# Kernel optimization log

Hardware: AMD Instinct MI355X
Metric: run time of the kernel (lower is better)

## Reference

```python
import jax, jax.numpy as jnp
import numpy as np

B, S, D, H, DK = 8, 1024, 768, 12, 64


def setup_inputs() -> dict:
    key = jax.random.key(0)
    k1, k2, k3, k4, k5 = jax.random.split(key, 5)
    return {
        "x": jax.random.normal(k1, (B, S, D), dtype=jnp.float32),
        "Wq": jax.random.normal(k2, (H, D, DK), dtype=jnp.float32),
        "Wk": jax.random.normal(k3, (H, D, DK), dtype=jnp.float32),
        "Wv": jax.random.normal(k4, (H, D, DK), dtype=jnp.float32),
        "W": jax.random.normal(k5, (D, D), dtype=jnp.float32),
    }


def reference(x, Wq, Wk, Wv, W):
    # Batched equivalent of the per-head SelfAttention loop + concat + W matmul.
    q = jnp.einsum("bsd,hdk->bhsk", x, Wq)  # [B,H,S,DK]
    k = jnp.einsum("bsd,hdk->bhsk", x, Wk)
    v = jnp.einsum("bsd,hdk->bhsk", x, Wv)
    scale = 1.0 / jnp.sqrt(jnp.asarray(DK, dtype=x.dtype))
    scores = jnp.einsum("bhsk,bhtk->bhst", q, k) * scale  # [B,H,S,S]
    attn = jax.nn.softmax(scores, axis=-1)
    z = jnp.einsum("bhst,bhtk->bhsk", attn, v)  # [B,H,S,DK]
    # concat heads along last dim: [B,S,H*DK]
    z = jnp.transpose(z, (0, 2, 1, 3)).reshape(x.shape[0], x.shape[1], H * DK)
    return jnp.matmul(z, W)  # [B,S,D]
```

## Files before the change

kernel.cpp:

```cpp
#include <hip/hip_runtime.h>

#define Bv 8
#define Sv 1024
#define Dv 768
#define Hv 12
#define DKv 64
#define Mv (Bv*Sv)
#define NQKV (3*Hv*DKv)
#define NQK (2*Hv*DKv)

typedef __attribute__((ext_vector_type(8))) short short8;
typedef __attribute__((ext_vector_type(4))) float f32x4;

__device__ __forceinline__ short f2bf(float f) {
    unsigned u = __builtin_bit_cast(unsigned, f);
    u += 0x7fffu + ((u >> 16) & 1u);
    return (short)(u >> 16);
}
__device__ __forceinline__ float bf2f(short h) {
    return __builtin_bit_cast(float, (unsigned)(unsigned short)h << 16);
}

__device__ __forceinline__ f32x4 mfma16(short8 a, short8 b, f32x4 c) {
    return __builtin_amdgcn_mfma_f32_16x16x32_bf16(a, b, c, 0, 0, 0);
}

__device__ __forceinline__ void gload16(const short* g, const short* l) {
    __builtin_amdgcn_global_load_lds(
        (const __attribute__((address_space(1))) unsigned int*)g,
        (__attribute__((address_space(3))) unsigned int*)(short*)l, 16, 0, 0);
}

__global__ void split_x_kernel(const float* __restrict__ x, short* __restrict__ xh,
                               short* __restrict__ xl) {
    int t = blockIdx.x * 256 + threadIdx.x;
    const float4* f = (const float4*)x + (size_t)t * 2;
    float4 a = f[0], b = f[1];
    float v[8] = {a.x,a.y,a.z,a.w,b.x,b.y,b.z,b.w};
    short8 oh, ol;
#pragma unroll
    for (int k = 0; k < 8; k++) {
        short hi = f2bf(v[k]);
        oh[k] = hi;
        ol[k] = f2bf(v[k] - bf2f(hi));
    }
    *((short8*)xh + t) = oh;
    *((short8*)xl + t) = ol;
}

__global__ void pack_wqkv_kernel(const float* __restrict__ Wq, const float* __restrict__ Wk,
                                 const float* __restrict__ Wv, short* __restrict__ Wh,
                                 short* __restrict__ Wl) {
    int dt = blockIdx.x;
    int h  = blockIdx.y;
    int p  = blockIdx.z;
    const float* S = (p == 0 ? Wq : (p == 1 ? Wk : Wv)) + (size_t)h * Dv * DKv;
    float sc = (p == 0) ? 0.125f : 1.0f;
    __shared__ float lds[64][65];
    int t = threadIdx.x;
    int d0 = dt * 64;
#pragma unroll
    for (int i = 0; i < 4; i++) {
        int v = t + i * 256;
        int r = v >> 4, c4 = v & 15;
        float4 f = *(const float4*)&S[(size_t)(d0 + r) * DKv + c4 * 4];
        lds[r][c4*4+0] = f.x; lds[r][c4*4+1] = f.y; lds[r][c4*4+2] = f.z; lds[r][c4*4+3] = f.w;
    }
    __syncthreads();
#pragma unroll
    for (int i = 0; i < 2; i++) {
        int v = t + i * 256;
        int kk = v >> 3, dl0 = (v & 7) * 8;
        short8 oh, ol;
#pragma unroll
        for (int k = 0; k < 8; k++) {
            float f = lds[dl0 + k][kk] * sc;
            short hi = f2bf(f);
            oh[k] = hi;
            ol[k] = f2bf(f - bf2f(hi));
        }
        size_t base = (size_t)(p*768 + h*64 + kk) * Dv + d0 + dl0;
        *(short8*)&Wh[base] = oh;
        if (p < 2) *(short8*)&Wl[base] = ol;
    }
}

__global__ void transpose_cast_kernel(const float* __restrict__ S, int S_cols,
                                      short* __restrict__ D, int D_ld) {
    int c0 = blockIdx.x * 64, r0 = blockIdx.y * 64;
    __shared__ float lds[64][65];
    int t = threadIdx.x;
#pragma unroll
    for (int i = 0; i < 4; i++) {
        int v = t + i * 256;
        int r = v >> 4, c4 = v & 15;
        float4 f = *(const float4*)&S[(size_t)(r0 + r) * S_cols + c0 + c4 * 4];
        lds[r][c4*4+0] = f.x; lds[r][c4*4+1] = f.y; lds[r][c4*4+2] = f.z; lds[r][c4*4+3] = f.w;
    }
    __syncthreads();
#pragma unroll
    for (int i = 0; i < 2; i++) {
        int v = t + i * 256;
        int oc = v >> 3, rl0 = (v & 7) * 8;
        short8 o;
#pragma unroll
        for (int k = 0; k < 8; k++) o[k] = f2bf(lds[rl0 + k][oc]);
        *(short8*)&D[(size_t)(c0 + oc) * D_ld + r0 + rl0] = o;
    }
}

__global__ void vtrans_kernel(const short* __restrict__ QKVh, short* __restrict__ Vt) {
    int sc = blockIdx.x;
    int bh = blockIdx.y;
    int b = bh / Hv, h = bh % Hv;
    __shared__ __align__(16) short lds[64][72];
    int t = threadIdx.x;
    int s0 = sc * 64;
#pragma unroll
    for (int i = 0; i < 2; i++) {
        int v = t + i * 256;
        int sl = v >> 3, c0 = (v & 7) * 8;
        short8 xv = *(const short8*)&QKVh[(size_t)(b*Sv + s0 + sl) * NQKV + NQK + h*DKv + c0];
        *(short8*)&lds[sl][c0] = xv;
    }
    __syncthreads();
#pragma unroll
    for (int i = 0; i < 2; i++) {
        int v = t + i * 256;
        int dk = v >> 3, tl0 = (v & 7) * 8;
        short8 o;
#pragma unroll
        for (int k = 0; k < 8; k++) o[k] = lds[tl0 + k][dk];
        *(short8*)&Vt[(size_t)(bh*64 + dk) * Sv + s0 + tl0] = o;
    }
}

__device__ __forceinline__ void swz_xy(int n, int& xbl, int& ybl) {
    int cx = n & 7, k = n >> 3;
    ybl = cx + 8 * (k & 7);
    xbl = k >> 3;
}

__global__ __launch_bounds__(256, 4) void gemm1_kernel(const short* __restrict__ xh,
                                                       const short* __restrict__ xl,
                                                       const short* __restrict__ Wh,
                                                       const short* __restrict__ Wl,
                                                       short* __restrict__ QKVh,
                                                       short* __restrict__ QKVl) {
    int xbl, ybl;
    swz_xy(blockIdx.x, xbl, ybl);
    int m0 = ybl * 128, n0 = xbl * 128;
    bool isv = (n0 >= NQK);
    int KT = isv ? 24 : 72;
    __shared__ __align__(16) short lA[2][4096];
    __shared__ __align__(16) short lB[2][4096];
    int tid = threadIdx.x, lane = tid & 63, w = tid >> 6;
    int wr = w >> 1, wc = w & 1;
    int li = lane & 15, g = lane >> 4;
    f32x4 zero = {0.f, 0.f, 0.f, 0.f};
    f32x4 acc[4][4];
#pragma unroll
    for (int i = 0; i < 4; i++)
#pragma unroll
        for (int j = 0; j < 4; j++) acc[i][j] = zero;

    int e0 = tid * 8;
    int sr0 = e0 >> 5;
    int sc0 = ((e0 >> 3) & 3) ^ ((sr0 >> 1) & 3);
    int sr1 = sr0 + 64;
    int sc1 = ((e0 >> 3) & 3) ^ ((sr1 >> 1) & 3);

    auto stage = [&](int t, int buf) {
        int seg = (t >= 48) ? 2 : (t >= 24 ? 1 : 0);
        int kk = (t - seg * 24) * 32;
        const short* Ab = (seg == 2) ? xl : xh;
        const short* Bb = (seg == 1) ? Wl : Wh;
        gload16(Ab + (size_t)(m0 + sr0) * Dv + kk + sc0 * 8, &lA[buf][w * 512]);
        gload16(Bb + (size_t)(n0 + sr0) * Dv + kk + sc0 * 8, &lB[buf][w * 512]);
        gload16(Ab + (size_t)(m0 + sr1) * Dv + kk + sc1 * 8, &lA[buf][2048 + w * 512]);
        gload16(Bb + (size_t)(n0 + sr1) * Dv + kk + sc1 * 8, &lB[buf][2048 + w * 512]);
    };

    stage(0, 0);
    stage(1, 1);

    for (int t = 0; t < KT; t++) {
        int cur = t & 1;
        if (t + 1 < KT) asm volatile("s_waitcnt vmcnt(4)" ::: "memory");
        else            asm volatile("s_waitcnt vmcnt(0)" ::: "memory");
        __builtin_amdgcn_s_barrier();
        __builtin_amdgcn_sched_barrier(0);
        short8 a[4], bb[4];
#pragma unroll
        for (int mi = 0; mi < 4; mi++) {
            int row = wr*64 + mi*16 + li;
            a[mi] = *(const short8*)&lA[cur][row * 32 + ((g ^ ((row >> 1) & 3)) << 3)];
        }
#pragma unroll
        for (int ni = 0; ni < 4; ni++) {
            int row = wc*64 + ni*16 + li;
            bb[ni] = *(const short8*)&lB[cur][row * 32 + ((g ^ ((row >> 1) & 3)) << 3)];
        }
#pragma unroll
        for (int mi = 0; mi < 4; mi++)
#pragma unroll
            for (int ni = 0; ni < 4; ni++)
                acc[mi][ni] = mfma16(a[mi], bb[ni], acc[mi][ni]);
        __builtin_amdgcn_sched_barrier(0);
        __builtin_amdgcn_s_barrier();
        __builtin_amdgcn_sched_barrier(0);
        if (t + 2 < KT) stage(t + 2, cur);
    }
#pragma unroll
    for (int mi = 0; mi < 4; mi++)
#pragma unroll
        for (int ni = 0; ni < 4; ni++)
#pragma unroll
            for (int j = 0; j < 4; j++) {
                int row = m0 + wr*64 + mi*16 + g*4 + j;
                int col = n0 + wc*64 + ni*16 + li;
                float v = acc[mi][ni][j];
                short hi = f2bf(v);
                QKVh[(size_t)row * NQKV + col] = hi;
                if (!isv) QKVl[(size_t)row * NQK + col] = f2bf(v - bf2f(hi));
            }
}

__global__ __launch_bounds__(256, 4) void gemm2_kernel(const short* __restrict__ A,
                                                       const short* __restrict__ Bt,
                                                       float* __restrict__ C) {
    int xbl, ybl;
    swz_xy(blockIdx.x, xbl, ybl);
    int m0 = ybl * 128, n0 = xbl * 128;
    __shared__ __align__(16) short lA[2][4096];
    __shared__ __align__(16) short lB[2][4096];
    int tid = threadIdx.x, lane = tid & 63, w = tid >> 6;
    int wr = w >> 1, wc = w & 1;
    int li = lane & 15, g = lane >> 4;
    f32x4 zero = {0.f, 0.f, 0.f, 0.f};
    f32x4 acc[4][4];
#pragma unroll
    for (int i = 0; i < 4; i++)
#pragma unroll
        for (int j = 0; j < 4; j++) acc[i][j] = zero;

    int e0 = tid * 8;
    int sr0 = e0 >> 5;
    int sc0 = ((e0 >> 3) & 3) ^ ((sr0 >> 1) & 3);
    int sr1 = sr0 + 64;
    int sc1 = ((e0 >> 3) & 3) ^ ((sr1 >> 1) & 3);

    auto stage = [&](int t, int buf) {
        int kk = t * 32;
        gload16(A  + (size_t)(m0 + sr0) * Dv + kk + sc0 * 8, &lA[buf][w * 512]);
        gload16(Bt + (size_t)(n0 + sr0) * Dv + kk + sc0 * 8, &lB[buf][w * 512]);
        gload16(A  + (size_t)(m0 + sr1) * Dv + kk + sc1 * 8, &lA[buf][2048 + w * 512]);
        gload16(Bt + (size_t)(n0 + sr1) * Dv + kk + sc1 * 8, &lB[buf][2048 + w * 512]);
    };

    stage(0, 0);
    stage(1, 1);

    for (int t = 0; t < 24; t++) {
        int cur = t & 1;
        if (t + 1 < 24) asm volatile("s_waitcnt vmcnt(4)" ::: "memory");
        else            asm volatile("s_waitcnt vmcnt(0)" ::: "memory");
        __builtin_amdgcn_s_barrier();
        __builtin_amdgcn_sched_barrier(0);
        short8 a[4], bb[4];
#pragma unroll
        for (int mi = 0; mi < 4; mi++) {
            int row = wr*64 + mi*16 + li;
            a[mi] = *(const short8*)&lA[cur][row * 32 + ((g ^ ((row >> 1) & 3)) << 3)];
        }
#pragma unroll
        for (int ni = 0; ni < 4; ni++) {
            int row = wc*64 + ni*16 + li;
            bb[ni] = *(const short8*)&lB[cur][row * 32 + ((g ^ ((row >> 1) & 3)) << 3)];
        }
#pragma unroll
        for (int mi = 0; mi < 4; mi++)
#pragma unroll
            for (int ni = 0; ni < 4; ni++)
                acc[mi][ni] = mfma16(a[mi], bb[ni], acc[mi][ni]);
        __builtin_amdgcn_sched_barrier(0);
        __builtin_amdgcn_s_barrier();
        __builtin_amdgcn_sched_barrier(0);
        if (t + 2 < 24) stage(t + 2, cur);
    }
#pragma unroll
    for (int mi = 0; mi < 4; mi++)
#pragma unroll
        for (int ni = 0; ni < 4; ni++)
#pragma unroll
            for (int j = 0; j < 4; j++) {
                int row = m0 + wr*64 + mi*16 + g*4 + j;
                int col = n0 + wc*64 + ni*16 + li;
                C[(size_t)row * Dv + col] = acc[mi][ni][j];
            }
}

__global__ __launch_bounds__(512, 6) void attn_kernel(const short* __restrict__ QKVh,
                                                      const short* __restrict__ QKVl,
                                                      const short* __restrict__ Vt,
                                                      short* __restrict__ Z) {
    int n = blockIdx.x;
    int j2 = n >> 3;
    int bh = (n & 7) + 8 * (j2 >> 3);
    int qb = j2 & 7;
    int b = bh / Hv, h = bh % Hv;
    int tid = threadIdx.x, lane = tid & 63, w = tid >> 6;
    int li = lane & 15, g = lane >> 4;

    __shared__ __align__(16) short Kh[64 * 64];
    __shared__ __align__(16) short Kl[64 * 64];
    __shared__ __align__(16) short Vs[64 * 64];
    __shared__ __align__(16) short P[8][1024];
    char* Pw = (char*)&P[w][0];
    const char* Khc = (const char*)Kh;
    const char* Klc = (const char*)Kl;
    const char* Vsc = (const char*)Vs;

    int qr0 = qb * 128 + w * 16;
    const short* qhr = QKVh + (size_t)(b*Sv + qr0 + li) * NQKV + h * DKv;
    const short* qlr = QKVl + (size_t)(b*Sv + qr0 + li) * NQK  + h * DKv;
    short8 qh0 = *(const short8*)(qhr + g * 8);
    short8 qh1 = *(const short8*)(qhr + 32 + g * 8);
    short8 ql0 = *(const short8*)(qlr + g * 8);
    short8 ql1 = *(const short8*)(qlr + 32 + g * 8);

    const short* Khb = QKVh + (size_t)(b*Sv) * NQKV + Hv*DKv + h*DKv;
    const short* Klb = QKVl + (size_t)(b*Sv) * NQK  + Hv*DKv + h*DKv;
    const short* Vbase = Vt + (size_t)(bh * 64) * Sv;

    int srow = w * 8 + (lane >> 3);
    int scs  = (lane & 7) ^ (srow & 7);

    float mm = -1e30f, ll = 0.f;
    f32x4 zero = {0.f, 0.f, 0.f, 0.f};
    f32x4 acc[4];
#pragma unroll
    for (int ni = 0; ni < 4; ni++) acc[ni] = zero;

    for (int t = 0; t < 16; t++) {
        int t0 = t * 64;
        gload16(Khb + (size_t)(t0 + srow) * NQKV + scs * 8, &Kh[w * 512]);
        gload16(Klb + (size_t)(t0 + srow) * NQK  + scs * 8, &Kl[w * 512]);
        gload16(Vbase + (size_t)srow * Sv + t0 + scs * 8,   &Vs[w * 512]);
        __syncthreads();

        f32x4 s[4];
#pragma unroll
        for (int tn = 0; tn < 4; tn++) {
            int row = tn * 16 + li;
            int rb = row * 128, rs = (row & 7) << 4;
            short8 kh0 = *(const short8*)(Khc + rb + ((g << 4) ^ rs));
            short8 kh1 = *(const short8*)(Khc + rb + ((64 + (g << 4)) ^ rs));
            short8 kl0 = *(const short8*)(Klc + rb + ((g << 4) ^ rs));
            short8 kl1 = *(const short8*)(Klc + rb + ((64 + (g << 4)) ^ rs));
            f32x4 z = mfma16(kh0, qh0, zero);
            z = mfma16(kh1, qh1, z);
            z = mfma16(kl0, qh0, z);
            z = mfma16(kl1, qh1, z);
            z = mfma16(kh0, ql0, z);
            z = mfma16(kh1, ql1, z);
            s[tn] = z;
        }
        float rm = s[0][0];
#pragma unroll
        for (int tn = 0; tn < 4; tn++)
#pragma unroll
            for (int jj = 0; jj < 4; jj++) rm = fmaxf(rm, s[tn][jj]);
        rm = fmaxf(rm, __shfl_xor(rm, 16));
        rm = fmaxf(rm, __shfl_xor(rm, 32));
        float mn = fmaxf(mm, rm);
        float sfu = __expf(mm - mn);
        float p[4][4];
        float rs2 = 0.f;
#pragma unroll
        for (int tn = 0; tn < 4; tn++)
#pragma unroll
            for (int jj = 0; jj < 4; jj++) { p[tn][jj] = __expf(s[tn][jj] - mn); rs2 += p[tn][jj]; }
        rs2 += __shfl_xor(rs2, 16);
        rs2 += __shfl_xor(rs2, 32);
        ll = ll * sfu + rs2;
        mm = mn;

        float sfq[4];
#pragma unroll
        for (int jj = 0; jj < 4; jj++) sfq[jj] = __shfl(sfu, g * 4 + jj);
#pragma unroll
        for (int ni = 0; ni < 4; ni++)
#pragma unroll
            for (int jj = 0; jj < 4; jj++) acc[ni][jj] *= sfq[jj];

#pragma unroll
        for (int tn = 0; tn < 4; tn++) {
            unsigned lo, hi;
            asm("v_cvt_pk_bf16_f32 %0, %1, %2" : "=v"(lo) : "v"(p[tn][0]), "v"(p[tn][1]));
            asm("v_cvt_pk_bf16_f32 %0, %1, %2" : "=v"(hi) : "v"(p[tn][2]), "v"(p[tn][3]));
            unsigned long long pk = (unsigned long long)lo | ((unsigned long long)hi << 32);
            int off = (li * 128 + tn * 32 + g * 8) ^ ((li & 7) << 4);
            *(unsigned long long*)(Pw + off) = pk;
        }
#pragma unroll
        for (int kt = 0; kt < 2; kt++) {
            int roff = (li * 128 + kt * 64 + g * 16) ^ ((li & 7) << 4);
            short8 ap = *(const short8*)(Pw + roff);
#pragma unroll
            for (int ni = 0; ni < 4; ni++) {
                int dk = ni * 16 + li;
                int vb = dk * 128 + ((((kt * 4 + g) << 4)) ^ ((dk & 7) << 4));
                short8 bv = *(const short8*)(Vsc + vb);
                acc[ni] = mfma16(ap, bv, acc[ni]);
            }
        }
        __syncthreads();
    }
    float inv = 1.f / ll;
    float invq[4];
#pragma unroll
    for (int jj = 0; jj < 4; jj++) invq[jj] = __shfl(inv, g * 4 + jj);
#pragma unroll
    for (int ni = 0; ni < 4; ni++)
#pragma unroll
        for (int jj = 0; jj < 4; jj++) {
            int row = b*Sv + qr0 + g*4 + jj;
            int col = h*DKv + ni*16 + li;
            Z[(size_t)row * Dv + col] = f2bf(acc[ni][jj] * invq[jj]);
        }
}

extern "C" void kernel_launch(void* const* d_in, const int* in_sizes, int n_in,
                              void* d_out, int out_size, void* d_ws, size_t ws_size,
                              hipStream_t stream) {
    const float* x  = (const float*)d_in[0];
    const float* Wq = (const float*)d_in[1];
    const float* Wk = (const float*)d_in[2];
    const float* Wv = (const float*)d_in[3];
    const float* W  = (const float*)d_in[4];
    float* out = (float*)d_out;

    short* xh   = (short*)d_ws;
    short* xl   = xh   + (size_t)Mv * Dv;
    short* Wh   = xl   + (size_t)Mv * Dv;
    short* Wl   = Wh   + (size_t)NQKV * Dv;
    short* W2T  = Wl   + (size_t)NQKV * Dv;
    short* QKVh = W2T  + (size_t)Dv * Dv;
    short* QKVl = QKVh + (size_t)Mv * NQKV;
    short* Vt   = QKVl + (size_t)Mv * NQK;
    short* Zb   = Vt   + (size_t)Bv*Hv*DKv * Sv;

    split_x_kernel<<<dim3(Mv * Dv / (256 * 8)), 256, 0, stream>>>(x, xh, xl);
    pack_wqkv_kernel<<<dim3(Dv/64, Hv, 3), 256, 0, stream>>>(Wq, Wk, Wv, Wh, Wl);
    transpose_cast_kernel<<<dim3(Dv/64, Dv/64), 256, 0, stream>>>(W, Dv, W2T, Dv);
    gemm1_kernel<<<dim3((NQKV/128) * (Mv/128)), 256, 0, stream>>>(xh, xl, Wh, Wl, QKVh, QKVl);
    vtrans_kernel<<<dim3(Sv/64, Bv*Hv), 256, 0, stream>>>(QKVh, Vt);
    attn_kernel<<<dim3(768), 512, 0, stream>>>(QKVh, QKVl, Vt, Zb);
    gemm2_kernel<<<dim3((Dv/128) * (Mv/128)), 256, 0, stream>>>(Zb, W2T, out);
}
```

Baseline: 203.4 us.

## Merge prep kernels into one launch and fuse V transpose into QKV GEMM epilogue

Three preprocessing kernels (x hi/lo split, Wqkv packing, W transpose-cast) are merged into one launch that dispatches on block index. The separate V transpose kernel is removed: the QKV GEMM epilogue for V tiles now writes bf16 results straight into the transposed Vt layout as 4-element vectors, so V is never written to QKVh and never re-read. This removes two kernel launches and a full read/write pass over V. In exchange, the Vt stores are narrow 8-byte writes at a stride of one sequence row, which may coalesce worse than the old epilogue stores.

```diff
diff --git a/kernel.cpp b/kernel.cpp
--- a/kernel.cpp
+++ b/kernel.cpp
@@ -10,6 +10,7 @@
 #define NQK (2*Hv*DKv)
 
 typedef __attribute__((ext_vector_type(8))) short short8;
+typedef __attribute__((ext_vector_type(4))) short short4v;
 typedef __attribute__((ext_vector_type(4))) float f32x4;
 
 __device__ __forceinline__ short f2bf(float f) {
@@ -31,107 +32,81 @@
         (__attribute__((address_space(3))) unsigned int*)(short*)l, 16, 0, 0);
 }
 
-__global__ void split_x_kernel(const float* __restrict__ x, short* __restrict__ xh,
-                               short* __restrict__ xl) {
-    int t = blockIdx.x * 256 + threadIdx.x;
-    const float4* f = (const float4*)x + (size_t)t * 2;
-    float4 a = f[0], b = f[1];
-    float v[8] = {a.x,a.y,a.z,a.w,b.x,b.y,b.z,b.w};
-    short8 oh, ol;
-#pragma unroll
-    for (int k = 0; k < 8; k++) {
-        short hi = f2bf(v[k]);
-        oh[k] = hi;
-        ol[k] = f2bf(v[k] - bf2f(hi));
-    }
-    *((short8*)xh + t) = oh;
-    *((short8*)xl + t) = ol;
-}
-
-__global__ void pack_wqkv_kernel(const float* __restrict__ Wq, const float* __restrict__ Wk,
-                                 const float* __restrict__ Wv, short* __restrict__ Wh,
-                                 short* __restrict__ Wl) {
-    int dt = blockIdx.x;
-    int h  = blockIdx.y;
-    int p  = blockIdx.z;
-    const float* S = (p == 0 ? Wq : (p == 1 ? Wk : Wv)) + (size_t)h * Dv * DKv;
-    float sc = (p == 0) ? 0.125f : 1.0f;
+__global__ __launch_bounds__(256) void prep_kernel(const float* __restrict__ x,
+                                                   const float* __restrict__ Wq,
+                                                   const float* __restrict__ Wk,
+                                                   const float* __restrict__ Wv,
+                                                   const float* __restrict__ W,
+                                                   short* __restrict__ xh, short* __restrict__ xl,
+                                                   short* __restrict__ Wh, short* __restrict__ Wl,
+                                                   short* __restrict__ W2T) {
     __shared__ float lds[64][65];
+    int bid = blockIdx.x;
     int t = threadIdx.x;
-    int d0 = dt * 64;
-#pragma unroll
-    for (int i = 0; i < 4; i++) {
-        int v = t + i * 256;
-        int r = v >> 4, c4 = v & 15;
-        float4 f = *(const float4*)&S[(size_t)(d0 + r) * DKv + c4 * 4];
-        lds[r][c4*4+0] = f.x; lds[r][c4*4+1] = f.y; lds[r][c4*4+2] = f.z; lds[r][c4*4+3] = f.w;
-    }
-    __syncthreads();
-#pragma unroll
-    for (int i = 0; i < 2; i++) {
-        int v = t + i * 256;
-        int kk = v >> 3, dl0 = (v & 7) * 8;
+    if (bid < 3072) {
+        int idx = bid * 256 + t;
+        const float4* f = (const float4*)x + (size_t)idx * 2;
+        float4 a = f[0], b = f[1];
+        float v[8] = {a.x,a.y,a.z,a.w,b.x,b.y,b.z,b.w};
         short8 oh, ol;
 #pragma unroll
         for (int k = 0; k < 8; k++) {
-            float f = lds[dl0 + k][kk] * sc;
-            short hi = f2bf(f);
+            short hi = f2bf(v[k]);
             oh[k] = hi;
-            ol[k] = f2bf(f - bf2f(hi));
-        }
-        size_t base = (size_t)(p*768 + h*64 + kk) * Dv + d0 + dl0;
-        *(short8*)&Wh[base] = oh;
-        if (p < 2) *(short8*)&Wl[base] = ol;
-    }
-}
-
-__global__ void transpose_cast_kernel(const float* __restrict__ S, int S_cols,
-                                      short* __restrict__ D, int D_ld) {
-    int c0 = blockIdx.x * 64, r0 = blockIdx.y * 64;
-    __shared__ float lds[64][65];
-    int t = threadIdx.x;
-#pragma unroll
-    for (int i = 0; i < 4; i++) {
-        int v = t + i * 256;
-        int r = v >> 4, c4 = v & 15;
-        float4 f = *(const float4*)&S[(size_t)(r0 + r) * S_cols + c0 + c4 * 4];
-        lds[r][c4*4+0] = f.x; lds[r][c4*4+1] = f.y; lds[r][c4*4+2] = f.z; lds[r][c4*4+3] = f.w;
-    }
-    __syncthreads();
-#pragma unroll
-    for (int i = 0; i < 2; i++) {
-        int v = t + i * 256;
-        int oc = v >> 3, rl0 = (v & 7) * 8;
-        short8 o;
-#pragma unroll
-        for (int k = 0; k < 8; k++) o[k] = f2bf(lds[rl0 + k][oc]);
-        *(short8*)&D[(size_t)(c0 + oc) * D_ld + r0 + rl0] = o;
-    }
-}
-
-__global__ void vtrans_kernel(const short* __restrict__ QKVh, short* __restrict__ Vt) {
-    int sc = blockIdx.x;
-    int bh = blockIdx.y;
-    int b = bh / Hv, h = bh % Hv;
-    __shared__ __align__(16) short lds[64][72];
-    int t = threadIdx.x;
-    int s0 = sc * 64;
-#pragma unroll
-    for (int i = 0; i < 2; i++) {
-        int v = t + i * 256;
-        int sl = v >> 3, c0 = (v & 7) * 8;
-        short8 xv = *(const short8*)&QKVh[(size_t)(b*Sv + s0 + sl) * NQKV + NQK + h*DKv + c0];
-        *(short8*)&lds[sl][c0] = xv;
-    }
-    __syncthreads();
-#pragma unroll
-    for (int i = 0; i < 2; i++) {
-        int v = t + i * 256;
-        int dk = v >> 3, tl0 = (v & 7) * 8;
-        short8 o;
-#pragma unroll
-        for (int k = 0; k < 8; k++) o[k] = lds[tl0 + k][dk];
-        *(short8*)&Vt[(size_t)(bh*64 + dk) * Sv + s0 + tl0] = o;
+            ol[k] = f2bf(v[k] - bf2f(hi));
+        }
+        *((short8*)xh + idx) = oh;
+        *((short8*)xl + idx) = ol;
+    } else if (bid < 3504) {
+        int idx = bid - 3072;
+        int dt = idx % 12, h = (idx / 12) % 12, p = idx / 144;
+        const float* S = (p == 0 ? Wq : (p == 1 ? Wk : Wv)) + (size_t)h * Dv * DKv;
+        float sc = (p == 0) ? 0.125f : 1.0f;
+        int d0 = dt * 64;
+#pragma unroll
+        for (int i = 0; i < 4; i++) {
+            int v = t + i * 256;
+            int r = v >> 4, c4 = v & 15;
+            float4 f = *(const float4*)&S[(size_t)(d0 + r) * DKv + c4 * 4];
+            lds[r][c4*4+0] = f.x; lds[r][c4*4+1] = f.y; lds[r][c4*4+2] = f.z; lds[r][c4*4+3] = f.w;
+        }
+        __syncthreads();
+#pragma unroll
+        for (int i = 0; i < 2; i++) {
+            int v = t + i * 256;
+            int kk = v >> 3, dl0 = (v & 7) * 8;
+            short8 oh, ol;
+#pragma unroll
+            for (int k = 0; k < 8; k++) {
+                float f = lds[dl0 + k][kk] * sc;
+                short hi = f2bf(f);
+                oh[k] = hi;
+                ol[k] = f2bf(f - bf2f(hi));
+            }
+            size_t base = (size_t)(p*768 + h*64 + kk) * Dv + d0 + dl0;
+            *(short8*)&Wh[base] = oh;
+            if (p < 2) *(short8*)&Wl[base] = ol;
+        }
+    } else {
+        int idx = bid - 3504;
+        int c0 = (idx % 12) * 64, r0 = (idx / 12) * 64;
+#pragma unroll
+        for (int i = 0; i < 4; i++) {
+            int v = t + i * 256;
+            int r = v >> 4, c4 = v & 15;
+            float4 f = *(const float4*)&W[(size_t)(r0 + r) * Dv + c0 + c4 * 4];
+            lds[r][c4*4+0] = f.x; lds[r][c4*4+1] = f.y; lds[r][c4*4+2] = f.z; lds[r][c4*4+3] = f.w;
+        }
+        __syncthreads();
+#pragma unroll
+        for (int i = 0; i < 2; i++) {
+            int v = t + i * 256;
+            int oc = v >> 3, rl0 = (v & 7) * 8;
+            short8 o;
+#pragma unroll
+            for (int k = 0; k < 8; k++) o[k] = f2bf(lds[rl0 + k][oc]);
+            *(short8*)&W2T[(size_t)(c0 + oc) * Dv + r0 + rl0] = o;
+        }
     }
 }
 
@@ -146,7 +121,8 @@
                                                        const short* __restrict__ Wh,
                                                        const short* __restrict__ Wl,
                                                        short* __restrict__ QKVh,
-                                                       short* __restrict__ QKVl) {
+                                                       short* __restrict__ QKVl,
+                                                       short* __restrict__ Vt) {
     int xbl, ybl;
     swz_xy(blockIdx.x, xbl, ybl);
     int m0 = ybl * 128, n0 = xbl * 128;
@@ -211,19 +187,35 @@
         __builtin_amdgcn_sched_barrier(0);
         if (t + 2 < KT) stage(t + 2, cur);
     }
-#pragma unroll
-    for (int mi = 0; mi < 4; mi++)
-#pragma unroll
-        for (int ni = 0; ni < 4; ni++)
-#pragma unroll
-            for (int j = 0; j < 4; j++) {
-                int row = m0 + wr*64 + mi*16 + g*4 + j;
-                int col = n0 + wc*64 + ni*16 + li;
-                float v = acc[mi][ni][j];
-                short hi = f2bf(v);
-                QKVh[(size_t)row * NQKV + col] = hi;
-                if (!isv) QKVl[(size_t)row * NQK + col] = f2bf(v - bf2f(hi));
+    if (isv) {
+#pragma unroll
+        for (int mi = 0; mi < 4; mi++)
+#pragma unroll
+            for (int ni = 0; ni < 4; ni++) {
+                int vcol = n0 + wc*64 + ni*16 + li - NQK;
+                int h = vcol >> 6, dk = vcol & 63;
+                int row0 = m0 + wr*64 + mi*16 + g*4;
+                int b = row0 >> 10, s0 = row0 & 1023;
+                short4v v4;
+                v4[0] = f2bf(acc[mi][ni][0]); v4[1] = f2bf(acc[mi][ni][1]);
+                v4[2] = f2bf(acc[mi][ni][2]); v4[3] = f2bf(acc[mi][ni][3]);
+                *(short4v*)&Vt[(size_t)((b*Hv + h)*64 + dk) * Sv + s0] = v4;
             }
+    } else {
+#pragma unroll
+        for (int mi = 0; mi < 4; mi++)
+#pragma unroll
+            for (int ni = 0; ni < 4; ni++)
+#pragma unroll
+                for (int j = 0; j < 4; j++) {
+                    int row = m0 + wr*64 + mi*16 + g*4 + j;
+                    int col = n0 + wc*64 + ni*16 + li;
+                    float v = acc[mi][ni][j];
+                    short hi = f2bf(v);
+                    QKVh[(size_t)row * NQKV + col] = hi;
+                    QKVl[(size_t)row * NQK + col] = f2bf(v - bf2f(hi));
+                }
+    }
 }
 
 __global__ __launch_bounds__(256, 4) void gemm2_kernel(const short* __restrict__ A,
@@ -451,11 +443,8 @@
     short* Vt   = QKVl + (size_t)Mv * NQK;
     short* Zb   = Vt   + (size_t)Bv*Hv*DKv * Sv;
 
-    split_x_kernel<<<dim3(Mv * Dv / (256 * 8)), 256, 0, stream>>>(x, xh, xl);
-    pack_wqkv_kernel<<<dim3(Dv/64, Hv, 3), 256, 0, stream>>>(Wq, Wk, Wv, Wh, Wl);
-    transpose_cast_kernel<<<dim3(Dv/64, Dv/64), 256, 0, stream>>>(W, Dv, W2T, Dv);
-    gemm1_kernel<<<dim3((NQKV/128) * (Mv/128)), 256, 0, stream>>>(xh, xl, Wh, Wl, QKVh, QKVl);
-    vtrans_kernel<<<dim3(Sv/64, Bv*Hv), 256, 0, stream>>>(QKVh, Vt);
+    prep_kernel<<<dim3(3648), 256, 0, stream>>>(x, Wq, Wk, Wv, W, xh, xl, Wh, Wl, W2T);
+    gemm1_kernel<<<dim3((NQKV/128) * (Mv/128)), 256, 0, stream>>>(xh, xl, Wh, Wl, QKVh, QKVl, Vt);
     attn_kernel<<<dim3(768), 512, 0, stream>>>(QKVh, QKVl, Vt, Zb);
     gemm2_kernel<<<dim3((Dv/128) * (Mv/128)), 256, 0, stream>>>(Zb, W2T, out);
 }
```

New measurement: 192.6 us (median of 2 runs). 1.06x faster.
